# Kernel optimization log

Hardware: AMD Instinct MI355X
Metric: run time of the kernel (lower is better)

## Reference

```python
import jax, jax.numpy as jnp
import numpy as np
from jax import lax

EPS = 1e-5
ALPHA = 100.0

def leaky_relu(x):
    return jnp.where(x >= 0, x, 0.2 * x)

def instance_norm(x):
    # per-sample, per-channel over (H, W), affine=False, eps=1e-5
    m = jnp.mean(x, axis=(2, 3), keepdims=True)
    v = jnp.var(x, axis=(2, 3), keepdims=True)
    return (x - m) / jnp.sqrt(v + EPS)

def conv2d(x, W, b, stride=1):
    y = lax.conv_general_dilated(x, W, (stride, stride), 'VALID',
                                 dimension_numbers=('NCHW', 'OIHW', 'NCHW'))
    return y + b[None, :, None, None]

def leaky_conv(x, W, b, pad, stride):
    # ReflectionPad2d(pad) -> Conv2d(pad=0) -> InstanceNorm -> LeakyReLU(0.2)
    if pad > 0:
        x = jnp.pad(x, ((0, 0), (0, 0), (pad, pad), (pad, pad)), mode='reflect')
    y = conv2d(x, W, b, stride)
    return leaky_relu(instance_norm(y))

def up2x_align_corners(x):
    # nn.UpsamplingBilinear2d(scale_factor=2) == bilinear with align_corners=True
    n, c, H, W = x.shape
    def coords(S):
        pos = jnp.arange(2 * S, dtype=x.dtype) * (S - 1) / (2 * S - 1)
        i0 = jnp.floor(pos).astype(jnp.int32)
        i1 = jnp.minimum(i0 + 1, S - 1)
        return i0, i1, pos - i0
    i0, i1, fh = coords(H)
    x = x[:, :, i0, :] * (1 - fh)[None, None, :, None] + x[:, :, i1, :] * fh[None, None, :, None]
    j0, j1, fw = coords(W)
    x = x[:, :, :, j0] * (1 - fw) + x[:, :, :, j1] * fw
    return x

def upsample_block(x, W, b):
    x = up2x_align_corners(x)
    # Conv2d(3,3,k=3,s=1,p=1) uses ZERO padding (plain nn.Conv2d padding arg)
    x = jnp.pad(x, ((0, 0), (0, 0), (1, 1), (1, 1)))
    return leaky_relu(instance_norm(conv2d(x, W, b)))

def cal_correlation(fa, fb, alpha):
    n, c, h, w = fa.shape
    fa = fa - jnp.mean(fa, axis=(2, 3), keepdims=True)
    fb = fb - jnp.mean(fb, axis=(2, 3), keepdims=True)
    fa = fa.reshape(n, c, h * w)
    fb = fb.reshape(n, c, h * w)
    fa = fa / (jnp.linalg.norm(fa, axis=1, keepdims=True) + EPS)
    fb = fb / (jnp.linalg.norm(fb, axis=1, keepdims=True) + EPS)
    energy = jnp.einsum('ncp,ncq->npq', fb, fa) * alpha  # [n, hw_b, hw_a]
    return jax.nn.softmax(energy, axis=1)

def setup_inputs() -> dict:
    key = jax.random.key(0)
    ks = jax.random.split(key, 16)
    C = 256
    d = {
        'fa_raw': jax.random.normal(ks[0], (2, C, 64, 64), jnp.float32),
        'fb_raw': jax.random.normal(ks[1], (2, C, 64, 64), jnp.float32),
        'fc_raw': jax.random.normal(ks[2], (2, 3, 256, 256), jnp.float32),
        'Wa': jax.random.normal(ks[3], (C // 4, C, 1, 1), jnp.float32) * 0.05,
        'ba': jnp.zeros((C // 4,), jnp.float32),
        'Wb': jax.random.normal(ks[4], (C // 4, C, 1, 1), jnp.float32) * 0.05,
        'bb': jnp.zeros((C // 4,), jnp.float32),
        'Wc1': jax.random.normal(ks[5], (3, 3, 3, 3), jnp.float32) * 0.2,
        'bc1': jnp.zeros((3,), jnp.float32),
        'Wc2': jax.random.normal(ks[6], (3, 3, 3, 3), jnp.float32) * 0.2,
        'bc2': jnp.zeros((3,), jnp.float32),
        'Wu1': jax.random.normal(ks[7], (3, 3, 3, 3), jnp.float32) * 0.2,
        'bu1': jnp.zeros((3,), jnp.float32),
        'Wu2': jax.random.normal(ks[8], (3, 3, 3, 3), jnp.float32) * 0.2,
        'bu2': jnp.zeros((3,), jnp.float32),
    }
    return d

def reference(fa_raw, fb_raw, fc_raw, Wa, ba, Wb, bb, Wc1, bc1, Wc2, bc2, Wu1, bu1, Wu2, bu2):
    fa = leaky_conv(fa_raw, Wa, ba, pad=0, stride=1)          # [n, 64, 64, 64]
    fb = leaky_conv(fb_raw, Wb, bb, pad=0, stride=1)
    fc = leaky_conv(fc_raw, Wc1, bc1, pad=1, stride=2)        # [n, 3, 128, 128]
    fc = leaky_conv(fc, Wc2, bc2, pad=1, stride=2)            # [n, 3, 64, 64]
    corr_ab_T = cal_correlation(fa, fb, ALPHA)                # [n, 4096, 4096]
    n, c, h, w = fc.shape
    fc_warp = jnp.einsum('ncp,npq->ncq', fc.reshape(n, c, h * w), corr_ab_T)
    fc_warp = fc_warp.reshape(n, c, h, w)
    fc_warp = upsample_block(fc_warp, Wu1, bu1)               # [n, 3, 128, 128]
    fc_warp = upsample_block(fc_warp, Wu2, bu2)               # [n, 3, 256, 256]
    return fc_warp, corr_ab_T
```

## Files before the change

kernel.cpp:

```cpp
#include <hip/hip_runtime.h>
#include <math.h>

#define EPS 1e-5f

typedef short short8 __attribute__((ext_vector_type(8)));
typedef __bf16 bf16x8 __attribute__((ext_vector_type(8)));
typedef float f32x4  __attribute__((ext_vector_type(4)));

__device__ __forceinline__ float lrelu(float x){ return x >= 0.f ? x : 0.2f*x; }

__device__ __forceinline__ short f2bf_s(float x){
    unsigned u = __float_as_uint(x);
    unsigned r = (u + 0x7FFFu + ((u >> 16) & 1u)) >> 16;
    return (short)r;
}
__device__ __forceinline__ float bfs2f(short h){
    return __uint_as_float(((unsigned)(unsigned short)h) << 16);
}

__device__ __forceinline__ f32x4 mfma16(bf16x8 a, bf16x8 b, f32x4 c){
    return __builtin_amdgcn_mfma_f32_16x16x32_bf16(a, b, c, 0, 0, 0);
}

__global__ __launch_bounds__(256,2) void feat_conv(
    const float* __restrict__ fa_raw, const float* __restrict__ fb_raw,
    const float* __restrict__ Wa, const float* __restrict__ Wb,
    const float* __restrict__ ba, const float* __restrict__ bb,
    float* __restrict__ Y, float* __restrict__ FSUM)
{
    __shared__ float wS[256*65];
    __shared__ float xS[16*64];

    int blk = blockIdx.x;
    int pch = blk & 63, n = (blk>>6)&1, side = blk>>7;
    int p0 = pch*64;
    const float* x    = (side ? fb_raw : fa_raw) + (size_t)n*256*4096 + p0;
    const float* W    = side ? Wb : Wa;
    const float* bias = side ? bb : ba;
    int tid = threadIdx.x;

    #pragma unroll
    for (int it=0; it<64; it++){
        int idx = it*256 + tid;
        int co = idx >> 8, ci = idx & 255;
        wS[ci*65 + co] = W[idx];
    }

    int pl = tid & 63, cog = tid >> 6;
    float acc[16];
    #pragma unroll
    for (int j=0;j<16;j++) acc[j] = 0.f;

    for (int cb=0; cb<16; cb++){
        __syncthreads();
        #pragma unroll
        for (int it=0; it<4; it++){
            int idx = it*256 + tid;
            int cl = idx >> 6, pp = idx & 63;
            xS[idx] = x[(size_t)(cb*16+cl)*4096 + pp];
        }
        __syncthreads();
        #pragma unroll
        for (int cl=0; cl<16; cl++){
            float xr = xS[cl*64 + pl];
            const float* wr = &wS[(cb*16+cl)*65 + cog*16];
            #pragma unroll
            for (int j=0;j<16;j++) acc[j] = fmaf(xr, wr[j], acc[j]);
        }
    }

    int pair = side*2 + n;
    #pragma unroll
    for (int j=0;j<16;j++){
        acc[j] += bias[cog*16+j];
        float v = acc[j], v2 = v*v;
        #pragma unroll
        for (int off=1; off<64; off<<=1){
            v  += __shfl_xor(v,  off);
            v2 += __shfl_xor(v2, off);
        }
        if (pl == 0){
            atomicAdd(&FSUM[(pair*64 + cog*16 + j)*2],   v);
            atomicAdd(&FSUM[(pair*64 + cog*16 + j)*2+1], v2);
        }
    }

    float* yr = Y + ((size_t)pair*4096 + p0 + pl)*64 + cog*16;
    #pragma unroll
    for (int j4=0;j4<4;j4++)
        *(float4*)(yr + j4*4) = make_float4(acc[j4*4],acc[j4*4+1],acc[j4*4+2],acc[j4*4+3]);
}

__global__ __launch_bounds__(256) void feat_apply(
    float* __restrict__ Y, const float* __restrict__ FSUM, float* __restrict__ M2SUM)
{
    __shared__ float red[256];
    int tid = threadIdx.x;
    size_t base = (size_t)blockIdx.x*4096;
    int pair = (int)(base >> 18);
    int co = tid & 63;
    int ch = pair*64 + co;
    float m   = FSUM[ch*2]   * (1.f/4096.f);
    float var = FSUM[ch*2+1] * (1.f/4096.f) - m*m;
    float inv = rsqrtf(var + EPS);
    float asum = 0.f;
    #pragma unroll
    for (int it=0; it<16; it++){
        size_t idx = base + it*256 + tid;
        float y2 = lrelu((Y[idx]-m)*inv);
        Y[idx] = y2;
        asum += y2;
    }
    red[tid] = asum; __syncthreads();
    if (tid < 64)
        atomicAdd(&M2SUM[pair*64 + tid], red[tid]+red[tid+64]+red[tid+128]+red[tid+192]);
}

__global__ void feat_finish(const float* __restrict__ Y, const float* __restrict__ M2SUM,
                            short* __restrict__ PK)
{
    int r = blockIdx.x*256 + threadIdx.x;
    int pair = r >> 12;
    int p = r & 4095;
    const float4* m4 = (const float4*)(M2SUM + pair*64);
    const float4* r4 = (const float4*)(Y + (size_t)r*64);
    float s = 0.f;
    float4 v[16];
    #pragma unroll
    for (int i=0;i<16;i++){
        float4 t = r4[i], mm = m4[i];
        t.x -= mm.x*(1.f/4096.f); t.y -= mm.y*(1.f/4096.f);
        t.z -= mm.z*(1.f/4096.f); t.w -= mm.w*(1.f/4096.f);
        v[i] = t;
        s += t.x*t.x + t.y*t.y + t.z*t.z + t.w*t.w;
    }
    float inv = 1.f/(sqrtf(s)+EPS);
    #pragma unroll
    for (int i=0;i<16;i++){ v[i].x*=inv; v[i].y*=inv; v[i].z*=inv; v[i].w*=inv; }

    int qb = p >> 7, rr = p & 127, g = rr >> 4, rl = rr & 15;
    short* blk = PK + (((size_t)pair*32 + qb) << 14);
    #pragma unroll
    for (int c=0;c<8;c++){
        float x[8] = {v[2*c].x, v[2*c].y, v[2*c].z, v[2*c].w,
                      v[2*c+1].x, v[2*c+1].y, v[2*c+1].z, v[2*c+1].w};
        short8 h, l;
        #pragma unroll
        for (int j=0;j<8;j++){
            short hh = f2bf_s(x[j]);
            h[j] = hh;
            l[j] = f2bf_s(x[j] - bfs2f(hh));
        }
        int idx = g*128 + c*16 + rl;
        *(short8*)(blk + idx*8)        = h;
        *(short8*)(blk + 8192 + idx*8) = l;
    }
}

template<int STRIDE, bool REFLECT>
__global__ void conv3_kernel(const float* __restrict__ in_, int H, int Wd,
                             const float* __restrict__ wgt,
                             const float* __restrict__ bias,
                             float* __restrict__ out, float* __restrict__ sums)
{
    int oH = (H-1)/STRIDE + 1, oW = (Wd-1)/STRIDE + 1;
    int tid = threadIdx.x;
    size_t idx = (size_t)blockIdx.x*256 + tid;
    int ow = (int)(idx % oW); size_t t = idx / oW;
    int oh = (int)(t % oH); t /= oH;
    int co = (int)(t % 3); int n = (int)(t/3);
    float w[27];
    #pragma unroll
    for (int i=0;i<27;i++) w[i] = wgt[co*27 + i];
    float acc = bias[co];
    #pragma unroll
    for (int ci=0;ci<3;ci++){
        size_t base = ((size_t)(n*3+ci))*H*Wd;
        #pragma unroll
        for (int kh=0;kh<3;kh++){
            int ih = oh*STRIDE + kh - 1;
            if (REFLECT) ih = ih<0 ? -ih : (ih>=H ? 2*H-2-ih : ih);
            #pragma unroll
            for (int kw=0;kw<3;kw++){
                int iw = ow*STRIDE + kw - 1;
                if (REFLECT) iw = iw<0 ? -iw : (iw>=Wd ? 2*Wd-2-iw : iw);
                bool ok = REFLECT || (ih>=0 && ih<H && iw>=0 && iw<Wd);
                if (ok) acc += w[(ci*3+kh)*3+kw] * in_[base + (size_t)ih*Wd + iw];
            }
        }
    }
    out[idx] = acc;
    __shared__ float red[256];
    red[tid] = acc; __syncthreads();
    for (int o=128;o>0;o>>=1){ if(tid<o) red[tid]+=red[tid+o]; __syncthreads(); }
    float blockSum = red[0]; __syncthreads();
    red[tid] = acc*acc; __syncthreads();
    for (int o=128;o>0;o>>=1){ if(tid<o) red[tid]+=red[tid+o]; __syncthreads(); }
    if (tid==0){
        int pair = n*3+co;
        atomicAdd(&sums[pair*2],   blockSum);
        atomicAdd(&sums[pair*2+1], red[0]);
    }
}

template<int H>
__global__ __launch_bounds__(256) void upconv3_kernel(
    const float* __restrict__ in_, const float* __restrict__ wgt,
    const float* __restrict__ bias, float* __restrict__ out,
    float* __restrict__ sums)
{
    const int oH = 2*H;
    int tid = threadIdx.x;
    size_t idx = (size_t)blockIdx.x*256 + tid;
    int ow = (int)(idx % oH); size_t t = idx / oH;
    int oh = (int)(t % oH); t /= oH;
    int co = (int)(t % 3); int n = (int)(t/3);

    float w[27];
    #pragma unroll
    for (int i=0;i<27;i++) w[i] = wgt[co*27 + i];

    int i0[3], i1[3], j0[3], j1[3];
    float fh[3], fw[3];
    bool vh[3], vw[3];
    #pragma unroll
    for (int k=0;k<3;k++){
        int ih = oh + k - 1;
        vh[k] = (ih>=0 && ih<oH);
        int ihc = vh[k] ? ih : 0;
        float ph = (float)ihc * (float)(H-1) / (float)(oH-1);
        i0[k] = (int)ph; i1[k] = min(i0[k]+1, H-1); fh[k] = ph - (float)i0[k];
        int iw = ow + k - 1;
        vw[k] = (iw>=0 && iw<oH);
        int iwc = vw[k] ? iw : 0;
        float pw = (float)iwc * (float)(H-1) / (float)(oH-1);
        j0[k] = (int)pw; j1[k] = min(j0[k]+1, H-1); fw[k] = pw - (float)j0[k];
    }

    float acc = bias[co];
    #pragma unroll
    for (int ci=0;ci<3;ci++){
        const float* p = in_ + ((size_t)(n*3+ci))*H*H;
        #pragma unroll
        for (int kh=0;kh<3;kh++){
            if (!vh[kh]) continue;
            const float* r0 = p + (size_t)i0[kh]*H;
            const float* r1 = p + (size_t)i1[kh]*H;
            #pragma unroll
            for (int kw=0;kw<3;kw++){
                if (!vw[kw]) continue;
                float v00=r0[j0[kw]], v01=r0[j1[kw]];
                float v10=r1[j0[kw]], v11=r1[j1[kw]];
                float v0 = v00 + (v01-v00)*fw[kw];
                float v1 = v10 + (v11-v10)*fw[kw];
                float u  = v0 + (v1-v0)*fh[kh];
                acc += w[(ci*3+kh)*3+kw] * u;
            }
        }
    }
    out[idx] = acc;
    __shared__ float red[256];
    red[tid] = acc; __syncthreads();
    for (int o=128;o>0;o>>=1){ if(tid<o) red[tid]+=red[tid+o]; __syncthreads(); }
    float blockSum = red[0]; __syncthreads();
    red[tid] = acc*acc; __syncthreads();
    for (int o=128;o>0;o>>=1){ if(tid<o) red[tid]+=red[tid+o]; __syncthreads(); }
    if (tid==0){
        int pair = n*3+co;
        atomicAdd(&sums[pair*2],   blockSum);
        atomicAdd(&sums[pair*2+1], red[0]);
    }
}

__global__ void inapply_kernel(const float* __restrict__ in, const float* __restrict__ sums,
                               int planeSize, float cntInv, float* __restrict__ out)
{
    size_t idx = (size_t)blockIdx.x*256 + threadIdx.x;
    int pair = (int)(idx / planeSize);
    float m = sums[pair*2]*cntInv;
    float v = sums[pair*2+1]*cntInv - m*m;
    float inv = rsqrtf(v + EPS);
    out[idx] = lrelu((in[idx]-m)*inv);
}

template<int PASS>
__global__ __launch_bounds__(256,2) void corr_mfma(
    const short* __restrict__ PK,
    float* __restrict__ corr, float* __restrict__ SSUM,
    const float* __restrict__ fc, float* __restrict__ WARP)
{
    __shared__ short lds[32768];

    int blk = blockIdx.x;
    int qb = blk & 31, pb = (blk >> 5) & 31, n = blk >> 10;
    int tid = threadIdx.x;

    const short* pkB = PK + (((size_t)(2+n)*32 + pb) << 14);
    const short* pkA = PK + (((size_t)( n )*32 + qb) << 14);
    #pragma unroll
    for (int it=0; it<16; it++){
        int cid = it*256 + tid;
        int side = cid >> 11;
        int off  = (cid & 2047)*8;
        short8 vv = *(const short8*)((side ? pkA : pkB) + off);
        *(short8*)(lds + side*16384 + off) = vv;
    }
    __syncthreads();

    int wave = tid >> 6, lane = tid & 63;
    int wp = wave >> 1, wq = wave & 1;
    int quad = lane >> 4, l16 = lane & 15;

    f32x4 acc[4][4];
    #pragma unroll
    for (int pt=0;pt<4;pt++)
        #pragma unroll
        for (int qt=0;qt<4;qt++)
            acc[pt][qt] = (f32x4){0.f,0.f,0.f,0.f};

    #pragma unroll
    for (int kc=0;kc<2;kc++){
        int cc = kc*4 + quad;
        bf16x8 Ah[4], Al[4], Bh[4], Bl[4];
        #pragma unroll
        for (int t4=0;t4<4;t4++){
            int offA = (((wp*4+t4)*8 + cc)*16 + l16)*8;
            Ah[t4] = (bf16x8)(*(const short8*)(lds + offA));
            Al[t4] = (bf16x8)(*(const short8*)(lds + 8192 + offA));
            int offB = 16384 + (((wq*4+t4)*8 + cc)*16 + l16)*8;
            Bh[t4] = (bf16x8)(*(const short8*)(lds + offB));
            Bl[t4] = (bf16x8)(*(const short8*)(lds + 8192 + offB));
        }
        #pragma unroll
        for (int pt=0;pt<4;pt++)
            #pragma unroll
            for (int qt=0;qt<4;qt++){
                acc[pt][qt] = mfma16(Ah[pt], Bh[qt], acc[pt][qt]);
                acc[pt][qt] = mfma16(Ah[pt], Bl[qt], acc[pt][qt]);
                acc[pt][qt] = mfma16(Al[pt], Bh[qt], acc[pt][qt]);
            }
    }

    if (PASS == 0){
        float colsum[4] = {0.f,0.f,0.f,0.f};
        #pragma unroll
        for (int pt=0;pt<4;pt++)
            #pragma unroll
            for (int qt=0;qt<4;qt++)
                #pragma unroll
                for (int i=0;i<4;i++)
                    colsum[qt] += __expf(fmaf(acc[pt][qt][i], 100.f, -64.f));
        #pragma unroll
        for (int qt=0;qt<4;qt++){
            float v = colsum[qt];
            v += __shfl_xor(v, 16);
            v += __shfl_xor(v, 32);
            if (lane < 16)
                atomicAdd(&SSUM[n*4096 + qb*128 + wq*64 + qt*16 + lane], v);
        }
    } else {
        float inv4[4];
        int qoff = n*4096 + qb*128 + wq*64 + l16;
        #pragma unroll
        for (int qt=0;qt<4;qt++) inv4[qt] = 1.f / SSUM[qoff + qt*16];
        float wa0[4]={0,0,0,0}, wa1[4]={0,0,0,0}, wa2[4]={0,0,0,0};
        const float* fcb = fc + (size_t)n*12288;
        float* corrN = corr + (size_t)n*4096*4096;
        #pragma unroll
        for (int pt=0;pt<4;pt++){
            #pragma unroll
            for (int i=0;i<4;i++){
                int p = pb*128 + wp*64 + pt*16 + quad*4 + i;
                float f0 = fcb[p], f1 = fcb[4096+p], f2 = fcb[8192+p];
                float* rowp = corrN + (size_t)p*4096 + qb*128 + wq*64 + l16;
                #pragma unroll
                for (int qt=0;qt<4;qt++){
                    float u = __expf(fmaf(acc[pt][qt][i], 100.f, -64.f)) * inv4[qt];
                    __builtin_nontemporal_store(u, &rowp[qt*16]);
                    wa0[qt] += f0*u; wa1[qt] += f1*u; wa2[qt] += f2*u;
                }
            }
        }
        #pragma unroll
        for (int qt=0;qt<4;qt++){
            float v0 = wa0[qt], v1 = wa1[qt], v2 = wa2[qt];
            v0 += __shfl_xor(v0,16); v0 += __shfl_xor(v0,32);
            v1 += __shfl_xor(v1,16); v1 += __shfl_xor(v1,32);
            v2 += __shfl_xor(v2,16); v2 += __shfl_xor(v2,32);
            if (lane < 16){
                int q = qb*128 + wq*64 + qt*16 + lane;
                atomicAdd(&WARP[(size_t)n*12288 +        q], v0);
                atomicAdd(&WARP[(size_t)n*12288 + 4096 + q], v1);
                atomicAdd(&WARP[(size_t)n*12288 + 8192 + q], v2);
            }
        }
    }
}

extern "C" void kernel_launch(void* const* d_in, const int* in_sizes, int n_in,
                              void* d_out, int out_size, void* d_ws, size_t ws_size,
                              hipStream_t stream)
{
    const float* fa_raw = (const float*)d_in[0];
    const float* fb_raw = (const float*)d_in[1];
    const float* fc_raw = (const float*)d_in[2];
    const float* Wa  = (const float*)d_in[3];
    const float* ba  = (const float*)d_in[4];
    const float* Wb  = (const float*)d_in[5];
    const float* bb  = (const float*)d_in[6];
    const float* Wc1 = (const float*)d_in[7];
    const float* bc1 = (const float*)d_in[8];
    const float* Wc2 = (const float*)d_in[9];
    const float* bc2 = (const float*)d_in[10];
    const float* Wu1 = (const float*)d_in[11];
    const float* bu1 = (const float*)d_in[12];
    const float* Wu2 = (const float*)d_in[13];
    const float* bu2 = (const float*)d_in[14];

    float* ws    = (float*)d_ws;
    float* FEAT  = ws;
    float* CONV1 = FEAT  + 1048576;
    float* FC64  = CONV1 + 98304;
    float* CONV2 = FC64  + 24576;
    float* CONV3 = CONV2 + 98304;
    float* SSUM  = CONV3 + 393216;
    float* SUMS  = SSUM  + 8192;
    float* FSUM  = SUMS  + 48;
    float* M2SUM = FSUM  + 512;
    float* WARP  = M2SUM + 256;
    short* PK    = (short*)(WARP + 24576);

    float* out_fc   = (float*)d_out;
    float* out_corr = out_fc + 393216;

    hipMemsetAsync(SSUM, 0, (size_t)(8192 + 48 + 512 + 256 + 24576)*sizeof(float), stream);

    feat_conv<<<256,256,0,stream>>>(fa_raw, fb_raw, Wa, Wb, ba, bb, FEAT, FSUM);
    feat_apply<<<256,256,0,stream>>>(FEAT, FSUM, M2SUM);
    feat_finish<<<64,256,0,stream>>>(FEAT, M2SUM, PK);

    conv3_kernel<2,true><<<384,256,0,stream>>>(fc_raw, 256,256, Wc1, bc1, CONV1, SUMS+0);
    inapply_kernel<<<384,256,0,stream>>>(CONV1, SUMS+0, 16384, 1.f/16384.f, CONV1);
    conv3_kernel<2,true><<<96,256,0,stream>>>(CONV1, 128,128, Wc2, bc2, FC64, SUMS+12);
    inapply_kernel<<<96,256,0,stream>>>(FC64, SUMS+12, 4096, 1.f/4096.f, FC64);

    corr_mfma<0><<<2048,256,0,stream>>>(PK, out_corr, SSUM, FC64, WARP);
    corr_mfma<1><<<2048,256,0,stream>>>(PK, out_corr, SSUM, FC64, WARP);

    upconv3_kernel<64><<<384,256,0,stream>>>(WARP, Wu1, bu1, CONV2, SUMS+24);
    inapply_kernel<<<384,256,0,stream>>>(CONV2, SUMS+24, 16384, 1.f/16384.f, CONV2);

    upconv3_kernel<128><<<1536,256,0,stream>>>(CONV2, Wu2, bu2, CONV3, SUMS+36);
    inapply_kernel<<<1536,256,0,stream>>>(CONV3, SUMS+36, 65536, 1.f/65536.f, out_fc);
}
```

Before: 365.3 us.

## Merge independent feature and fc conv stages into combined kernels, fold norms into consumers

Runs the 1x1 feature convolution and the first stride-2 fc convolution in a single launch by splitting on block index. The second fc convolution is merged with the feature-stat pass in the same way. Instance-norm plus LeakyReLU is no longer written back by separate apply kernels; each consumer (next conv, feat_finish, corr_mfma, second upconv) recomputes it from the accumulated sums. This drops several launches and full read/write passes over intermediates, at the cost of extra per-element arithmetic and a mega1 block that reserves the large shared buffer even on conv3 blocks.

New measurement: 386.5 us. 1.06x slower.

```diff
diff --git a/kernel.cpp b/kernel.cpp
--- a/kernel.cpp
+++ b/kernel.cpp
@@ -22,150 +22,16 @@
     return __builtin_amdgcn_mfma_f32_16x16x32_bf16(a, b, c, 0, 0, 0);
 }
 
-__global__ __launch_bounds__(256,2) void feat_conv(
-    const float* __restrict__ fa_raw, const float* __restrict__ fb_raw,
-    const float* __restrict__ Wa, const float* __restrict__ Wb,
-    const float* __restrict__ ba, const float* __restrict__ bb,
-    float* __restrict__ Y, float* __restrict__ FSUM)
-{
-    __shared__ float wS[256*65];
-    __shared__ float xS[16*64];
-
-    int blk = blockIdx.x;
-    int pch = blk & 63, n = (blk>>6)&1, side = blk>>7;
-    int p0 = pch*64;
-    const float* x    = (side ? fb_raw : fa_raw) + (size_t)n*256*4096 + p0;
-    const float* W    = side ? Wb : Wa;
-    const float* bias = side ? bb : ba;
-    int tid = threadIdx.x;
-
-    #pragma unroll
-    for (int it=0; it<64; it++){
-        int idx = it*256 + tid;
-        int co = idx >> 8, ci = idx & 255;
-        wS[ci*65 + co] = W[idx];
-    }
-
-    int pl = tid & 63, cog = tid >> 6;
-    float acc[16];
-    #pragma unroll
-    for (int j=0;j<16;j++) acc[j] = 0.f;
-
-    for (int cb=0; cb<16; cb++){
-        __syncthreads();
-        #pragma unroll
-        for (int it=0; it<4; it++){
-            int idx = it*256 + tid;
-            int cl = idx >> 6, pp = idx & 63;
-            xS[idx] = x[(size_t)(cb*16+cl)*4096 + pp];
-        }
-        __syncthreads();
-        #pragma unroll
-        for (int cl=0; cl<16; cl++){
-            float xr = xS[cl*64 + pl];
-            const float* wr = &wS[(cb*16+cl)*65 + cog*16];
-            #pragma unroll
-            for (int j=0;j<16;j++) acc[j] = fmaf(xr, wr[j], acc[j]);
-        }
-    }
-
-    int pair = side*2 + n;
-    #pragma unroll
-    for (int j=0;j<16;j++){
-        acc[j] += bias[cog*16+j];
-        float v = acc[j], v2 = v*v;
-        #pragma unroll
-        for (int off=1; off<64; off<<=1){
-            v  += __shfl_xor(v,  off);
-            v2 += __shfl_xor(v2, off);
-        }
-        if (pl == 0){
-            atomicAdd(&FSUM[(pair*64 + cog*16 + j)*2],   v);
-            atomicAdd(&FSUM[(pair*64 + cog*16 + j)*2+1], v2);
-        }
-    }
-
-    float* yr = Y + ((size_t)pair*4096 + p0 + pl)*64 + cog*16;
-    #pragma unroll
-    for (int j4=0;j4<4;j4++)
-        *(float4*)(yr + j4*4) = make_float4(acc[j4*4],acc[j4*4+1],acc[j4*4+2],acc[j4*4+3]);
-}
-
-__global__ __launch_bounds__(256) void feat_apply(
-    float* __restrict__ Y, const float* __restrict__ FSUM, float* __restrict__ M2SUM)
-{
-    __shared__ float red[256];
-    int tid = threadIdx.x;
-    size_t base = (size_t)blockIdx.x*4096;
-    int pair = (int)(base >> 18);
-    int co = tid & 63;
-    int ch = pair*64 + co;
-    float m   = FSUM[ch*2]   * (1.f/4096.f);
-    float var = FSUM[ch*2+1] * (1.f/4096.f) - m*m;
-    float inv = rsqrtf(var + EPS);
-    float asum = 0.f;
-    #pragma unroll
-    for (int it=0; it<16; it++){
-        size_t idx = base + it*256 + tid;
-        float y2 = lrelu((Y[idx]-m)*inv);
-        Y[idx] = y2;
-        asum += y2;
-    }
-    red[tid] = asum; __syncthreads();
-    if (tid < 64)
-        atomicAdd(&M2SUM[pair*64 + tid], red[tid]+red[tid+64]+red[tid+128]+red[tid+192]);
-}
-
-__global__ void feat_finish(const float* __restrict__ Y, const float* __restrict__ M2SUM,
-                            short* __restrict__ PK)
-{
-    int r = blockIdx.x*256 + threadIdx.x;
-    int pair = r >> 12;
-    int p = r & 4095;
-    const float4* m4 = (const float4*)(M2SUM + pair*64);
-    const float4* r4 = (const float4*)(Y + (size_t)r*64);
-    float s = 0.f;
-    float4 v[16];
-    #pragma unroll
-    for (int i=0;i<16;i++){
-        float4 t = r4[i], mm = m4[i];
-        t.x -= mm.x*(1.f/4096.f); t.y -= mm.y*(1.f/4096.f);
-        t.z -= mm.z*(1.f/4096.f); t.w -= mm.w*(1.f/4096.f);
-        v[i] = t;
-        s += t.x*t.x + t.y*t.y + t.z*t.z + t.w*t.w;
-    }
-    float inv = 1.f/(sqrtf(s)+EPS);
-    #pragma unroll
-    for (int i=0;i<16;i++){ v[i].x*=inv; v[i].y*=inv; v[i].z*=inv; v[i].w*=inv; }
-
-    int qb = p >> 7, rr = p & 127, g = rr >> 4, rl = rr & 15;
-    short* blk = PK + (((size_t)pair*32 + qb) << 14);
-    #pragma unroll
-    for (int c=0;c<8;c++){
-        float x[8] = {v[2*c].x, v[2*c].y, v[2*c].z, v[2*c].w,
-                      v[2*c+1].x, v[2*c+1].y, v[2*c+1].z, v[2*c+1].w};
-        short8 h, l;
-        #pragma unroll
-        for (int j=0;j<8;j++){
-            short hh = f2bf_s(x[j]);
-            h[j] = hh;
-            l[j] = f2bf_s(x[j] - bfs2f(hh));
-        }
-        int idx = g*128 + c*16 + rl;
-        *(short8*)(blk + idx*8)        = h;
-        *(short8*)(blk + 8192 + idx*8) = l;
-    }
-}
-
-template<int STRIDE, bool REFLECT>
-__global__ void conv3_kernel(const float* __restrict__ in_, int H, int Wd,
-                             const float* __restrict__ wgt,
-                             const float* __restrict__ bias,
-                             float* __restrict__ out, float* __restrict__ sums)
+template<int STRIDE, bool REFLECT, bool NORM>
+__device__ __forceinline__ void conv3_unit(
+    int u, const float* __restrict__ in_, int H, int Wd,
+    const float* __restrict__ wgt, const float* __restrict__ bias,
+    const float* __restrict__ nsum, float cntInv,
+    float* __restrict__ out, float* __restrict__ sums, float* red)
 {
     int oH = (H-1)/STRIDE + 1, oW = (Wd-1)/STRIDE + 1;
     int tid = threadIdx.x;
-    size_t idx = (size_t)blockIdx.x*256 + tid;
+    size_t idx = (size_t)u*256 + tid;
     int ow = (int)(idx % oW); size_t t = idx / oW;
     int oh = (int)(t % oH); t /= oH;
     int co = (int)(t % 3); int n = (int)(t/3);
@@ -175,6 +41,13 @@
     float acc = bias[co];
     #pragma unroll
     for (int ci=0;ci<3;ci++){
+        float mm = 0.f, iv = 0.f;
+        if (NORM){
+            int pr = n*3+ci;
+            float m_ = nsum[pr*2]*cntInv;
+            float v_ = nsum[pr*2+1]*cntInv - m_*m_;
+            mm = m_; iv = rsqrtf(v_ + EPS);
+        }
         size_t base = ((size_t)(n*3+ci))*H*Wd;
         #pragma unroll
         for (int kh=0;kh<3;kh++){
@@ -185,12 +58,15 @@
                 int iw = ow*STRIDE + kw - 1;
                 if (REFLECT) iw = iw<0 ? -iw : (iw>=Wd ? 2*Wd-2-iw : iw);
                 bool ok = REFLECT || (ih>=0 && ih<H && iw>=0 && iw<Wd);
-                if (ok) acc += w[(ci*3+kh)*3+kw] * in_[base + (size_t)ih*Wd + iw];
+                if (ok){
+                    float val = in_[base + (size_t)ih*Wd + iw];
+                    if (NORM) val = lrelu((val-mm)*iv);
+                    acc += w[(ci*3+kh)*3+kw] * val;
+                }
             }
         }
     }
     out[idx] = acc;
-    __shared__ float red[256];
     red[tid] = acc; __syncthreads();
     for (int o=128;o>0;o>>=1){ if(tid<o) red[tid]+=red[tid+o]; __syncthreads(); }
     float blockSum = red[0]; __syncthreads();
@@ -201,17 +77,19 @@
         atomicAdd(&sums[pair*2],   blockSum);
         atomicAdd(&sums[pair*2+1], red[0]);
     }
-}
-
-template<int H>
-__global__ __launch_bounds__(256) void upconv3_kernel(
-    const float* __restrict__ in_, const float* __restrict__ wgt,
-    const float* __restrict__ bias, float* __restrict__ out,
-    float* __restrict__ sums)
+    __syncthreads();
+}
+
+template<int H, bool NORM>
+__device__ __forceinline__ void upconv3_unit(
+    int u, const float* __restrict__ in_,
+    const float* __restrict__ wgt, const float* __restrict__ bias,
+    const float* __restrict__ nsum, float cntInv,
+    float* __restrict__ out, float* __restrict__ sums, float* red)
 {
     const int oH = 2*H;
     int tid = threadIdx.x;
-    size_t idx = (size_t)blockIdx.x*256 + tid;
+    size_t idx = (size_t)u*256 + tid;
     int ow = (int)(idx % oH); size_t t = idx / oH;
     int oh = (int)(t % oH); t /= oH;
     int co = (int)(t % 3); int n = (int)(t/3);
@@ -240,6 +118,13 @@
     float acc = bias[co];
     #pragma unroll
     for (int ci=0;ci<3;ci++){
+        float mm = 0.f, iv = 0.f;
+        if (NORM){
+            int pr = n*3+ci;
+            float m_ = nsum[pr*2]*cntInv;
+            float v_ = nsum[pr*2+1]*cntInv - m_*m_;
+            mm = m_; iv = rsqrtf(v_ + EPS);
+        }
         const float* p = in_ + ((size_t)(n*3+ci))*H*H;
         #pragma unroll
         for (int kh=0;kh<3;kh++){
@@ -251,15 +136,18 @@
                 if (!vw[kw]) continue;
                 float v00=r0[j0[kw]], v01=r0[j1[kw]];
                 float v10=r1[j0[kw]], v11=r1[j1[kw]];
+                if (NORM){
+                    v00 = lrelu((v00-mm)*iv); v01 = lrelu((v01-mm)*iv);
+                    v10 = lrelu((v10-mm)*iv); v11 = lrelu((v11-mm)*iv);
+                }
                 float v0 = v00 + (v01-v00)*fw[kw];
                 float v1 = v10 + (v11-v10)*fw[kw];
-                float u  = v0 + (v1-v0)*fh[kh];
-                acc += w[(ci*3+kh)*3+kw] * u;
+                float uu = v0 + (v1-v0)*fh[kh];
+                acc += w[(ci*3+kh)*3+kw] * uu;
             }
         }
     }
     out[idx] = acc;
-    __shared__ float red[256];
     red[tid] = acc; __syncthreads();
     for (int o=128;o>0;o>>=1){ if(tid<o) red[tid]+=red[tid+o]; __syncthreads(); }
     float blockSum = red[0]; __syncthreads();
@@ -270,6 +158,180 @@
         atomicAdd(&sums[pair*2],   blockSum);
         atomicAdd(&sums[pair*2+1], red[0]);
     }
+    __syncthreads();
+}
+
+__global__ __launch_bounds__(256,2) void mega1(
+    const float* __restrict__ fa_raw, const float* __restrict__ fb_raw,
+    const float* __restrict__ Wa, const float* __restrict__ Wb,
+    const float* __restrict__ ba, const float* __restrict__ bb,
+    float* __restrict__ Y, float* __restrict__ FSUM,
+    const float* __restrict__ fc_raw,
+    const float* __restrict__ Wc1, const float* __restrict__ bc1,
+    float* __restrict__ CONV1, float* __restrict__ SUMS)
+{
+    __shared__ float sh[17664];
+    int blk = blockIdx.x, tid = threadIdx.x;
+
+    if (blk < 256){
+        int pch = blk & 63, n = (blk>>6)&1, side = blk>>7;
+        int p0 = pch*64;
+        const float* x    = (side ? fb_raw : fa_raw) + (size_t)n*256*4096 + p0;
+        const float* W    = side ? Wb : Wa;
+        const float* bias = side ? bb : ba;
+        float* wS = sh;
+        float* xS = sh + 16640;
+
+        #pragma unroll
+        for (int it=0; it<64; it++){
+            int idx = it*256 + tid;
+            int co = idx >> 8, ci = idx & 255;
+            wS[ci*65 + co] = W[idx];
+        }
+
+        int pl = tid & 63, cog = tid >> 6;
+        float acc[16];
+        #pragma unroll
+        for (int j=0;j<16;j++) acc[j] = 0.f;
+
+        for (int cb=0; cb<16; cb++){
+            __syncthreads();
+            #pragma unroll
+            for (int it=0; it<4; it++){
+                int idx = it*256 + tid;
+                int cl = idx >> 6, pp = idx & 63;
+                xS[idx] = x[(size_t)(cb*16+cl)*4096 + pp];
+            }
+            __syncthreads();
+            #pragma unroll
+            for (int cl=0; cl<16; cl++){
+                float xr = xS[cl*64 + pl];
+                const float* wr = &wS[(cb*16+cl)*65 + cog*16];
+                #pragma unroll
+                for (int j=0;j<16;j++) acc[j] = fmaf(xr, wr[j], acc[j]);
+            }
+        }
+
+        int pair = side*2 + n;
+        #pragma unroll
+        for (int j=0;j<16;j++){
+            acc[j] += bias[cog*16+j];
+            float v = acc[j], v2 = v*v;
+            #pragma unroll
+            for (int off=1; off<64; off<<=1){
+                v  += __shfl_xor(v,  off);
+                v2 += __shfl_xor(v2, off);
+            }
+            if (pl == 0){
+                atomicAdd(&FSUM[(pair*64 + cog*16 + j)*2],   v);
+                atomicAdd(&FSUM[(pair*64 + cog*16 + j)*2+1], v2);
+            }
+        }
+
+        float* yr = Y + ((size_t)pair*4096 + p0 + pl)*64 + cog*16;
+        #pragma unroll
+        for (int j4=0;j4<4;j4++)
+            *(float4*)(yr + j4*4) = make_float4(acc[j4*4],acc[j4*4+1],acc[j4*4+2],acc[j4*4+3]);
+    } else {
+        conv3_unit<2,true,false>(blk-256, fc_raw, 256,256, Wc1, bc1, nullptr, 0.f,
+                                 CONV1, SUMS, sh);
+    }
+}
+
+__global__ __launch_bounds__(256) void mega2(
+    const float* __restrict__ Y, const float* __restrict__ FSUM,
+    float* __restrict__ M2SUM,
+    const float* __restrict__ CONV1,
+    const float* __restrict__ Wc2, const float* __restrict__ bc2,
+    float* __restrict__ SUMS, float* __restrict__ FC64,
+    float* __restrict__ FSTm, float* __restrict__ FSTi)
+{
+    __shared__ float red[256];
+    int blk = blockIdx.x, tid = threadIdx.x;
+
+    if (blk < 256){
+        size_t base = (size_t)blk*4096;
+        int pair = blk >> 6;
+        int co = tid & 63;
+        int ch = pair*64 + co;
+        float m   = FSUM[ch*2]   * (1.f/4096.f);
+        float var = FSUM[ch*2+1] * (1.f/4096.f) - m*m;
+        float inv = rsqrtf(var + EPS);
+        float asum = 0.f;
+        #pragma unroll
+        for (int it=0; it<16; it++){
+            size_t idx = base + it*256 + tid;
+            asum += lrelu((Y[idx]-m)*inv);
+        }
+        red[tid] = asum; __syncthreads();
+        if (tid < 64)
+            atomicAdd(&M2SUM[pair*64 + tid], red[tid]+red[tid+64]+red[tid+128]+red[tid+192]);
+    } else if (blk < 352){
+        conv3_unit<2,true,true>(blk-256, CONV1, 128,128, Wc2, bc2, SUMS+0, 1.f/16384.f,
+                                FC64, SUMS+12, red);
+    } else {
+        int ch = tid;
+        float m   = FSUM[ch*2]   * (1.f/4096.f);
+        float var = FSUM[ch*2+1] * (1.f/4096.f) - m*m;
+        FSTm[ch] = m;
+        FSTi[ch] = rsqrtf(var + EPS);
+    }
+}
+
+__global__ void feat_finish(const float* __restrict__ Y, const float* __restrict__ M2SUM,
+                            const float* __restrict__ FSTm, const float* __restrict__ FSTi,
+                            short* __restrict__ PK)
+{
+    int r = blockIdx.x*256 + threadIdx.x;
+    int pair = r >> 12;
+    int p = r & 4095;
+    const float4* m4  = (const float4*)(M2SUM + pair*64);
+    const float4* cm4 = (const float4*)(FSTm + pair*64);
+    const float4* ci4 = (const float4*)(FSTi + pair*64);
+    const float4* r4  = (const float4*)(Y + (size_t)r*64);
+    float s = 0.f;
+    float4 v[16];
+    #pragma unroll
+    for (int i=0;i<16;i++){
+        float4 t = r4[i], mm = m4[i], cm = cm4[i], ci = ci4[i];
+        t.x = lrelu((t.x-cm.x)*ci.x) - mm.x*(1.f/4096.f);
+        t.y = lrelu((t.y-cm.y)*ci.y) - mm.y*(1.f/4096.f);
+        t.z = lrelu((t.z-cm.z)*ci.z) - mm.z*(1.f/4096.f);
+        t.w = lrelu((t.w-cm.w)*ci.w) - mm.w*(1.f/4096.f);
+        v[i] = t;
+        s += t.x*t.x + t.y*t.y + t.z*t.z + t.w*t.w;
+    }
+    float inv = 1.f/(sqrtf(s)+EPS);
+    #pragma unroll
+    for (int i=0;i<16;i++){ v[i].x*=inv; v[i].y*=inv; v[i].z*=inv; v[i].w*=inv; }
+
+    int qb = p >> 7, rr = p & 127, g = rr >> 4, rl = rr & 15;
+    short* blk = PK + (((size_t)pair*32 + qb) << 14);
+    #pragma unroll
+    for (int c=0;c<8;c++){
+        float x[8] = {v[2*c].x, v[2*c].y, v[2*c].z, v[2*c].w,
+                      v[2*c+1].x, v[2*c+1].y, v[2*c+1].z, v[2*c+1].w};
+        short8 h, l;
+        #pragma unroll
+        for (int j=0;j<8;j++){
+            short hh = f2bf_s(x[j]);
+            h[j] = hh;
+            l[j] = f2bf_s(x[j] - bfs2f(hh));
+        }
+        int idx = g*128 + c*16 + rl;
+        *(short8*)(blk + idx*8)        = h;
+        *(short8*)(blk + 8192 + idx*8) = l;
+    }
+}
+
+template<int H, bool NORM>
+__global__ __launch_bounds__(256) void upconv3_kernel(
+    const float* __restrict__ in_, const float* __restrict__ wgt,
+    const float* __restrict__ bias, const float* __restrict__ nsum, float cntInv,
+    float* __restrict__ out, float* __restrict__ sums)
+{
+    __shared__ float red[256];
+    upconv3_unit<H,NORM>(blockIdx.x, in_, wgt, bias, nsum, cntInv, out, sums, red);
 }
 
 __global__ void inapply_kernel(const float* __restrict__ in, const float* __restrict__ sums,
@@ -287,7 +349,8 @@
 __global__ __launch_bounds__(256,2) void corr_mfma(
     const short* __restrict__ PK,
     float* __restrict__ corr, float* __restrict__ SSUM,
-    const float* __restrict__ fc, float* __restrict__ WARP)
+    const float* __restrict__ FC64, const float* __restrict__ fsums,
+    float* __restrict__ WARP)
 {
     __shared__ short lds[32768];
 
@@ -363,15 +426,26 @@
         int qoff = n*4096 + qb*128 + wq*64 + l16;
         #pragma unroll
         for (int qt=0;qt<4;qt++) inv4[qt] = 1.f / SSUM[qoff + qt*16];
+
+        float fm[3], fiv[3];
+        #pragma unroll
+        for (int c=0;c<3;c++){
+            float m_ = fsums[(n*3+c)*2]   * (1.f/4096.f);
+            float v_ = fsums[(n*3+c)*2+1] * (1.f/4096.f) - m_*m_;
+            fm[c] = m_; fiv[c] = rsqrtf(v_ + EPS);
+        }
+
         float wa0[4]={0,0,0,0}, wa1[4]={0,0,0,0}, wa2[4]={0,0,0,0};
-        const float* fcb = fc + (size_t)n*12288;
+        const float* fcb = FC64 + (size_t)n*12288;
         float* corrN = corr + (size_t)n*4096*4096;
         #pragma unroll
         for (int pt=0;pt<4;pt++){
             #pragma unroll
             for (int i=0;i<4;i++){
                 int p = pb*128 + wp*64 + pt*16 + quad*4 + i;
-                float f0 = fcb[p], f1 = fcb[4096+p], f2 = fcb[8192+p];
+                float f0 = lrelu((fcb[p]      -fm[0])*fiv[0]);
+                float f1 = lrelu((fcb[4096+p] -fm[1])*fiv[1]);
+                float f2 = lrelu((fcb[8192+p] -fm[2])*fiv[2]);
                 float* rowp = corrN + (size_t)p*4096 + qb*128 + wq*64 + l16;
                 #pragma unroll
                 for (int qt=0;qt<4;qt++){
@@ -428,28 +502,29 @@
     float* FSUM  = SUMS  + 48;
     float* M2SUM = FSUM  + 512;
     float* WARP  = M2SUM + 256;
-    short* PK    = (short*)(WARP + 24576);
+    float* FSTm  = WARP  + 24576;
+    float* FSTi  = FSTm  + 256;
+    short* PK    = (short*)(FSTi + 256);
 
     float* out_fc   = (float*)d_out;
     float* out_corr = out_fc + 393216;
 
     hipMemsetAsync(SSUM, 0, (size_t)(8192 + 48 + 512 + 256 + 24576)*sizeof(float), stream);
 
-    feat_conv<<<256,256,0,stream>>>(fa_raw, fb_raw, Wa, Wb, ba, bb, FEAT, FSUM);
-    feat_apply<<<256,256,0,stream>>>(FEAT, FSUM, M2SUM);
-    feat_finish<<<64,256,0,stream>>>(FEAT, M2SUM, PK);
-
-    conv3_kernel<2,true><<<384,256,0,stream>>>(fc_raw, 256,256, Wc1, bc1, CONV1, SUMS+0);
-    inapply_kernel<<<384,256,0,stream>>>(CONV1, SUMS+0, 16384, 1.f/16384.f, CONV1);
-    conv3_kernel<2,true><<<96,256,0,stream>>>(CONV1, 128,128, Wc2, bc2, FC64, SUMS+12);
-    inapply_kernel<<<96,256,0,stream>>>(FC64, SUMS+12, 4096, 1.f/4096.f, FC64);
-
-    corr_mfma<0><<<2048,256,0,stream>>>(PK, out_corr, SSUM, FC64, WARP);
-    corr_mfma<1><<<2048,256,0,stream>>>(PK, out_corr, SSUM, FC64, WARP);
-
-    upconv3_kernel<64><<<384,256,0,stream>>>(WARP, Wu1, bu1, CONV2, SUMS+24);
-    inapply_kernel<<<384,256,0,stream>>>(CONV2, SUMS+24, 16384, 1.f/16384.f, CONV2);
-
-    upconv3_kernel<128><<<1536,256,0,stream>>>(CONV2, Wu2, bu2, CONV3, SUMS+36);
+    mega1<<<640,256,0,stream>>>(fa_raw, fb_raw, Wa, Wb, ba, bb, FEAT, FSUM,
+                                fc_raw, Wc1, bc1, CONV1, SUMS+0);
+
+    mega2<<<353,256,0,stream>>>(FEAT, FSUM, M2SUM, CONV1, Wc2, bc2, SUMS, FC64,
+                                FSTm, FSTi);
+
+    feat_finish<<<64,256,0,stream>>>(FEAT, M2SUM, FSTm, FSTi, PK);
+
+    corr_mfma<0><<<2048,256,0,stream>>>(PK, out_corr, SSUM, FC64, SUMS+12, WARP);
+    corr_mfma<1><<<2048,256,0,stream>>>(PK, out_corr, SSUM, FC64, SUMS+12, WARP);
+
+    upconv3_kernel<64,false><<<384,256,0,stream>>>(WARP, Wu1, bu1, nullptr, 0.f,
+                                                   CONV2, SUMS+24);
+    upconv3_kernel<128,true><<<1536,256,0,stream>>>(CONV2, Wu2, bu2, SUMS+24, 1.f/16384.f,
+                                                    CONV3, SUMS+36);
     inapply_kernel<<<1536,256,0,stream>>>(CONV3, SUMS+36, 65536, 1.f/65536.f, out_fc);
 }
```
